# Optimization experiments

Hardware: AMD Instinct MI355X
Metric: run time of the kernel (lower is better)

The kernel has to match this reference:

```python
import jax, jax.numpy as jnp
import numpy as np

HIDDEN = 1024
FFN = 4 * HIDDEN
NUM_EXPERTS = 8
TOP_K = 2
B, S = 4, 2048


def setup_inputs() -> dict:
    key = jax.random.key(0)
    ks = jax.random.split(key, 7)
    scale = 0.02
    return {
        "x": jax.random.normal(ks[0], (B, S, HIDDEN), dtype=jnp.float32),
        "gate_w": jax.random.normal(ks[1], (HIDDEN, NUM_EXPERTS), dtype=jnp.float32) * scale,
        "gate_b": jnp.zeros((NUM_EXPERTS,), dtype=jnp.float32),
        "w1": jax.random.normal(ks[2], (NUM_EXPERTS, HIDDEN, FFN), dtype=jnp.float32) * scale,
        "b1": jnp.zeros((NUM_EXPERTS, FFN), dtype=jnp.float32),
        "w2": jax.random.normal(ks[3], (NUM_EXPERTS, FFN, HIDDEN), dtype=jnp.float32) * scale,
        "b2": jnp.zeros((NUM_EXPERTS, HIDDEN), dtype=jnp.float32),
    }


def reference(x, gate_w, gate_b, w1, b1, w2, b2):
    b, s, h = x.shape
    xt = x.reshape(b * s, h)  # [T, H]
    # gate: Linear + softmax
    probs = jax.nn.softmax(xt @ gate_w + gate_b, axis=-1)  # [T, E]
    _, idx = jax.lax.top_k(probs, TOP_K)  # [T, K] int32
    # one-hot over top-k -> boolean per-expert mask (matches original one_hot.sum>0)
    one_hot = jax.nn.one_hot(idx, NUM_EXPERTS, dtype=xt.dtype)  # [T, K, E]
    mask = (one_hot.sum(axis=1) > 0).astype(xt.dtype)  # [T, E]
    # every expert MLP applied to all tokens (dense equivalent of gather-MLP-scatter),
    # then masked combine: output[t] = sum_e mask[t,e] * MLP_e(x[t])
    h1 = jax.nn.relu(jnp.einsum('th,ehf->etf', xt, w1) + b1[:, None, :])  # [E, T, F]
    out_e = jnp.einsum('etf,efh->eth', h1, w2) + b2[:, None, :]  # [E, T, H]
    out = jnp.einsum('eth,te->th', out_e, mask)  # [T, H]
    return out.reshape(b, s, h)
```

## Files before the change

### kernel.cpp

```cpp
#include <hip/hip_runtime.h>

typedef __bf16 bf16_t;
typedef bf16_t bf16x8 __attribute__((ext_vector_type(8)));
typedef bf16_t bf16x4 __attribute__((ext_vector_type(4)));
typedef float floatx4 __attribute__((ext_vector_type(4)));

#define T_TOKENS 8192
#define HIDDEN 1024
#define FFN 4096
#define NE 8
#define PAIRS 16384
#define NTILES 136

#define GLD16(gp, lp) __builtin_amdgcn_global_load_lds( \
    (const __attribute__((address_space(1))) void*)(gp), \
    (__attribute__((address_space(3))) void*)(lp), 16, 0, 0)

__global__ __launch_bounds__(256) void gate_kernel(
    const float* __restrict__ x, const float* __restrict__ gw,
    const float* __restrict__ gb, unsigned* __restrict__ top2,
    int* __restrict__ counts)
{
    const int lane = threadIdx.x & 63;
    const int wid  = threadIdx.x >> 6;
    const int t    = blockIdx.x * 4 + wid;
    const float* xr = x + (size_t)t * HIDDEN;

    float s[NE];
#pragma unroll
    for (int e = 0; e < NE; ++e) s[e] = 0.f;
    for (int k = lane; k < HIDDEN; k += 64) {
        float xv = xr[k];
        const float* g = gw + (size_t)k * NE;
#pragma unroll
        for (int e = 0; e < NE; ++e) s[e] += xv * g[e];
    }
#pragma unroll
    for (int e = 0; e < NE; ++e) {
#pragma unroll
        for (int off = 32; off > 0; off >>= 1) s[e] += __shfl_xor(s[e], off, 64);
    }
    if (lane == 0) {
        float v1 = -1e30f, v2 = -1e30f;
        int i1 = 0, i2 = 0;
#pragma unroll
        for (int e = 0; e < NE; ++e) {
            float v = s[e] + gb[e];
            if (v > v1)      { v2 = v1; i2 = i1; v1 = v; i1 = e; }
            else if (v > v2) { v2 = v;  i2 = e; }
        }
        top2[t] = (unsigned)(i1 | (i2 << 4));
        atomicAdd(&counts[i1], 1);
        atomicAdd(&counts[i2], 1);
    }
}

__global__ void offsets_kernel(const int* __restrict__ counts,
                               int* __restrict__ offs,
                               int* __restrict__ tinfo)
{
    int acc = 0, nt = 0;
    for (int e = 0; e < NE; ++e) {
        offs[e] = acc;
        int n = counts[e];
        for (int r = 0; r < n; r += 128) tinfo[nt++] = e | ((r >> 7) << 4);
        acc += n;
    }
    for (; nt < NTILES; ++nt) tinfo[nt] = (65535 << 4);
}

__global__ __launch_bounds__(256) void scatter_kernel(
    unsigned* __restrict__ top2_slots, const int* __restrict__ offs,
    int* __restrict__ fill, unsigned short* __restrict__ tok16)
{
    const int t = blockIdx.x * 256 + threadIdx.x;
    const unsigned v = top2_slots[t];
    const int e1 = v & 15, e2 = (v >> 4) & 15;
    int p1 = atomicAdd(&fill[e1], 1);
    int s1 = offs[e1] + p1;
    tok16[s1] = (unsigned short)t;
    int p2 = atomicAdd(&fill[e2], 1);
    int s2 = offs[e2] + p2;
    tok16[s2] = (unsigned short)t;
    top2_slots[t] = (unsigned)s1 | ((unsigned)s2 << 16);
}

__global__ __launch_bounds__(256) void xconv_kernel(
    const float* __restrict__ x, bf16_t* __restrict__ xb)
{
    size_t i = ((size_t)blockIdx.x * 256 + threadIdx.x) * 4;
    float4 v = *(const float4*)(x + i);
    bf16x4 b;
    b[0] = (bf16_t)v.x; b[1] = (bf16_t)v.y; b[2] = (bf16_t)v.z; b[3] = (bf16_t)v.w;
    *(bf16x4*)(xb + i) = b;
}

__global__ __launch_bounds__(256) void wtrans_kernel(
    const float* __restrict__ in, bf16_t* __restrict__ out, int R, int C)
{
    __shared__ bf16_t L[64][68];
    const int e  = blockIdx.z;
    const int r0 = blockIdx.y * 64;
    const int c0 = blockIdx.x * 64;
    const float* ip = in + ((size_t)e * R + r0) * C + c0;
    bf16_t* op = out + ((size_t)e * C + c0) * R + r0;
    const int tid = threadIdx.x;
    const int lr = tid >> 4, lc4 = tid & 15;
#pragma unroll
    for (int p = 0; p < 4; ++p) {
        int r = p * 16 + lr;
        float4 v = *(const float4*)(ip + (size_t)r * C + lc4 * 4);
        bf16x4 b;
        b[0] = (bf16_t)v.x; b[1] = (bf16_t)v.y; b[2] = (bf16_t)v.z; b[3] = (bf16_t)v.w;
        *(bf16x4*)&L[r][lc4 * 4] = b;
    }
    __syncthreads();
#pragma unroll
    for (int p = 0; p < 4; ++p) {
        int c  = p * 16 + lr;
        int rr = lc4 * 4;
        bf16x4 b;
        b[0] = L[rr + 0][c]; b[1] = L[rr + 1][c];
        b[2] = L[rr + 2][c]; b[3] = L[rr + 3][c];
        *(bf16x4*)(op + (size_t)c * R + rr) = b;
    }
}

__global__ __launch_bounds__(256) void moe_gemm1(
    const bf16_t* __restrict__ xb, const bf16_t* __restrict__ w1t,
    const float* __restrict__ b1, const int* __restrict__ counts,
    const int* __restrict__ offs, const unsigned short* __restrict__ tok16,
    const int* __restrict__ tinfo, bf16_t* __restrict__ h1)
{
    const int info = tinfo[blockIdx.y];
    const int e    = info & 15;
    const int row0 = (info >> 4) << 7;
    const int n_e  = counts[e];
    if (row0 >= n_e) return;
    const int seg   = offs[e];
    const int fcol0 = blockIdx.x * 128;

    __shared__ bf16_t As[128 * 32];
    __shared__ bf16_t Bs[128 * 32];

    const int tid  = threadIdx.x;
    const int wid  = tid >> 6, lane = tid & 63;
    const int wm   = wid & 1,  wn   = wid >> 1;
    const int quad = lane >> 4, lrow = lane & 15;

    const bf16_t* pA[2]; const bf16_t* pB[2];
#pragma unroll
    for (int q = 0; q < 2; ++q) {
        int slot = q * 256 + tid;
        int arow = slot >> 2, ko = slot & 3;
        int ridx = row0 + arow; if (ridx > n_e - 1) ridx = n_e - 1;
        pA[q] = xb + (size_t)tok16[seg + ridx] * HIDDEN + ko * 8;
        pB[q] = w1t + ((size_t)e * FFN + fcol0 + arow) * HIDDEN + ko * 8;
    }

    floatx4 acc[4][4];
#pragma unroll
    for (int i = 0; i < 4; ++i)
#pragma unroll
        for (int j = 0; j < 4; ++j) acc[i][j] = (floatx4){0.f, 0.f, 0.f, 0.f};

    for (int k0 = 0; k0 < HIDDEN; k0 += 32) {
#pragma unroll
        for (int q = 0; q < 2; ++q) {
            GLD16(pA[q], As + (q * 256 + wid * 64) * 8);
            GLD16(pB[q], Bs + (q * 256 + wid * 64) * 8);
            pA[q] += 32; pB[q] += 32;
        }
        __syncthreads();
        bf16x8 af[4], bfr[4];
#pragma unroll
        for (int mi = 0; mi < 4; ++mi)
            af[mi] = *(const bf16x8*)&As[(wm * 64 + mi * 16 + lrow) * 32 + quad * 8];
#pragma unroll
        for (int ni = 0; ni < 4; ++ni)
            bfr[ni] = *(const bf16x8*)&Bs[(wn * 64 + ni * 16 + lrow) * 32 + quad * 8];
#pragma unroll
        for (int mi = 0; mi < 4; ++mi)
#pragma unroll
            for (int ni = 0; ni < 4; ++ni)
                acc[mi][ni] = __builtin_amdgcn_mfma_f32_16x16x32_bf16(
                    af[mi], bfr[ni], acc[mi][ni], 0, 0, 0);
        __syncthreads();
    }

#pragma unroll
    for (int ni = 0; ni < 4; ++ni) {
        const int col = wn * 64 + ni * 16 + lrow;
        const float bias = b1[(size_t)e * FFN + fcol0 + col];
#pragma unroll
        for (int mi = 0; mi < 4; ++mi) {
#pragma unroll
            for (int r = 0; r < 4; ++r) {
                int row = wm * 64 + mi * 16 + quad * 4 + r;
                if (row0 + row < n_e) {
                    float v = acc[mi][ni][r] + bias;
                    v = v > 0.f ? v : 0.f;
                    h1[(size_t)(seg + row0 + row) * FFN + fcol0 + col] = (bf16_t)v;
                }
            }
        }
    }
}

__global__ __launch_bounds__(256) void moe_gemm2(
    const bf16_t* __restrict__ h1, const bf16_t* __restrict__ w2t,
    const float* __restrict__ b2, const int* __restrict__ counts,
    const int* __restrict__ offs, const int* __restrict__ tinfo,
    float* __restrict__ out_pairs)
{
    const int info = tinfo[blockIdx.y];
    const int e    = info & 15;
    const int row0 = (info >> 4) << 7;
    const int n_e  = counts[e];
    if (row0 >= n_e) return;
    const int seg   = offs[e];
    const int hcol0 = blockIdx.x * 128;

    __shared__ bf16_t As[128 * 32];
    __shared__ bf16_t Bs[128 * 32];

    const int tid  = threadIdx.x;
    const int wid  = tid >> 6, lane = tid & 63;
    const int wm   = wid & 1,  wn   = wid >> 1;
    const int quad = lane >> 4, lrow = lane & 15;

    const bf16_t* pA[2]; const bf16_t* pB[2];
#pragma unroll
    for (int q = 0; q < 2; ++q) {
        int slot = q * 256 + tid;
        int arow = slot >> 2, ko = slot & 3;
        int ridx = row0 + arow; if (ridx > n_e - 1) ridx = n_e - 1;
        pA[q] = h1 + (size_t)(seg + ridx) * FFN + ko * 8;
        pB[q] = w2t + ((size_t)e * HIDDEN + hcol0 + arow) * FFN + ko * 8;
    }

    floatx4 acc[4][4];
#pragma unroll
    for (int i = 0; i < 4; ++i)
#pragma unroll
        for (int j = 0; j < 4; ++j) acc[i][j] = (floatx4){0.f, 0.f, 0.f, 0.f};

    for (int k0 = 0; k0 < FFN; k0 += 32) {
#pragma unroll
        for (int q = 0; q < 2; ++q) {
            GLD16(pA[q], As + (q * 256 + wid * 64) * 8);
            GLD16(pB[q], Bs + (q * 256 + wid * 64) * 8);
            pA[q] += 32; pB[q] += 32;
        }
        __syncthreads();
        bf16x8 af[4], bfr[4];
#pragma unroll
        for (int mi = 0; mi < 4; ++mi)
            af[mi] = *(const bf16x8*)&As[(wm * 64 + mi * 16 + lrow) * 32 + quad * 8];
#pragma unroll
        for (int ni = 0; ni < 4; ++ni)
            bfr[ni] = *(const bf16x8*)&Bs[(wn * 64 + ni * 16 + lrow) * 32 + quad * 8];
#pragma unroll
        for (int mi = 0; mi < 4; ++mi)
#pragma unroll
            for (int ni = 0; ni < 4; ++ni)
                acc[mi][ni] = __builtin_amdgcn_mfma_f32_16x16x32_bf16(
                    af[mi], bfr[ni], acc[mi][ni], 0, 0, 0);
        __syncthreads();
    }

#pragma unroll
    for (int ni = 0; ni < 4; ++ni) {
        const int col = wn * 64 + ni * 16 + lrow;
        const float bias = b2[(size_t)e * HIDDEN + hcol0 + col];
#pragma unroll
        for (int mi = 0; mi < 4; ++mi) {
#pragma unroll
            for (int r = 0; r < 4; ++r) {
                int row = wm * 64 + mi * 16 + quad * 4 + r;
                if (row0 + row < n_e) {
                    out_pairs[(size_t)(seg + row0 + row) * HIDDEN + hcol0 + col] =
                        acc[mi][ni][r] + bias;
                }
            }
        }
    }
}

__global__ __launch_bounds__(256) void combine_kernel(
    const float* __restrict__ op, const unsigned* __restrict__ slots,
    float* __restrict__ out)
{
    const int gid = blockIdx.x * 256 + threadIdx.x;
    const int t = gid >> 8;
    const int c = (gid & 255) * 4;
    const unsigned sv = slots[t];
    const int s1 = sv & 0xffff, s2 = sv >> 16;
    float4 a = *(const float4*)(op + (size_t)s1 * HIDDEN + c);
    float4 b = *(const float4*)(op + (size_t)s2 * HIDDEN + c);
    float4 o;
    o.x = a.x + b.x; o.y = a.y + b.y; o.z = a.z + b.z; o.w = a.w + b.w;
    *(float4*)(out + (size_t)t * HIDDEN + c) = o;
}

extern "C" void kernel_launch(void* const* d_in, const int* in_sizes, int n_in,
                              void* d_out, int out_size, void* d_ws, size_t ws_size,
                              hipStream_t stream)
{
    const float* x      = (const float*)d_in[0];
    const float* gate_w = (const float*)d_in[1];
    const float* gate_b = (const float*)d_in[2];
    const float* w1     = (const float*)d_in[3];
    const float* b1     = (const float*)d_in[4];
    const float* w2     = (const float*)d_in[5];
    const float* b2     = (const float*)d_in[6];
    float* out = (float*)d_out;

    char* ws = (char*)d_ws;
    int*      counts = (int*)(ws + 0);
    int*      fill   = (int*)(ws + 32);
    int*      offs   = (int*)(ws + 64);
    int*      tinfo  = (int*)(ws + 96);
    unsigned* top2   = (unsigned*)(ws + 640);
    unsigned short* tok16 = (unsigned short*)(ws + 640 + 32768);
    const size_t o_base = 98560;

    const size_t sz_xb  = (size_t)T_TOKENS * HIDDEN * 2;
    const size_t sz_w1t = (size_t)NE * FFN * HIDDEN * 2;
    const size_t sz_w2t = (size_t)NE * HIDDEN * FFN * 2;
    const size_t sz_h1  = (size_t)PAIRS * FFN * 2;
    const size_t need = o_base + sz_xb + sz_w1t + sz_w2t + sz_h1;
    if (ws_size < need) return;

    bf16_t* xb  = (bf16_t*)(ws + o_base);
    bf16_t* w1t = (bf16_t*)(ws + o_base + sz_xb);
    bf16_t* w2t = (bf16_t*)(ws + o_base + sz_xb + sz_w1t);
    bf16_t* h1  = (bf16_t*)(ws + o_base + sz_xb + sz_w1t + sz_w2t);
    float* out_pairs = (float*)w1t;

    hipMemsetAsync(ws, 0, 96, stream);

    gate_kernel<<<T_TOKENS / 4, 256, 0, stream>>>(x, gate_w, gate_b, top2, counts);
    offsets_kernel<<<1, 1, 0, stream>>>(counts, offs, tinfo);
    scatter_kernel<<<T_TOKENS / 256, 256, 0, stream>>>(top2, offs, fill, tok16);

    xconv_kernel<<<(T_TOKENS * HIDDEN) / 1024, 256, 0, stream>>>(x, xb);
    wtrans_kernel<<<dim3(FFN / 64, HIDDEN / 64, NE), 256, 0, stream>>>(w1, w1t, HIDDEN, FFN);
    wtrans_kernel<<<dim3(HIDDEN / 64, FFN / 64, NE), 256, 0, stream>>>(w2, w2t, FFN, HIDDEN);

    moe_gemm1<<<dim3(FFN / 128, NTILES), 256, 0, stream>>>(
        xb, w1t, b1, counts, offs, tok16, tinfo, h1);
    moe_gemm2<<<dim3(HIDDEN / 128, NTILES), 256, 0, stream>>>(
        h1, w2t, b2, counts, offs, tinfo, out_pairs);
    combine_kernel<<<(T_TOKENS * HIDDEN / 4) / 256, 256, 0, stream>>>(
        out_pairs, top2, out);
}
```

Measured before the change: 1.128 ms.

## Fuse x conversion into gate, widen GEMM K tile, swizzle LDS, atomic combine

The bf16 conversion of x moves into the gate kernel, and the separate combine kernel is dropped: gemm2 atomically adds biased results straight into a zeroed output. Both GEMMs use a 64-wide K tile with an XOR-swizzled LDS layout to reduce bank conflicts, a remapped block order that groups tiles for cache reuse, and a 3-blocks-per-CU launch bound. gemm1 now stages its output through LDS for 16-byte coalesced stores. The float atomics make the summation order nondeterministic and add a full memset of the output.

```diff
diff --git a/kernel.cpp b/kernel.cpp
--- a/kernel.cpp
+++ b/kernel.cpp
@@ -11,6 +11,7 @@
 #define NE 8
 #define PAIRS 16384
 #define NTILES 136
+#define BK 64
 
 #define GLD16(gp, lp) __builtin_amdgcn_global_load_lds( \
     (const __attribute__((address_space(1))) void*)(gp), \
@@ -19,21 +20,31 @@
 __global__ __launch_bounds__(256) void gate_kernel(
     const float* __restrict__ x, const float* __restrict__ gw,
     const float* __restrict__ gb, unsigned* __restrict__ top2,
-    int* __restrict__ counts)
+    int* __restrict__ counts, bf16_t* __restrict__ xb)
 {
     const int lane = threadIdx.x & 63;
     const int wid  = threadIdx.x >> 6;
     const int t    = blockIdx.x * 4 + wid;
-    const float* xr = x + (size_t)t * HIDDEN;
+    const float4* xr = (const float4*)(x + (size_t)t * HIDDEN);
+    bf16_t* xo = xb + (size_t)t * HIDDEN;
 
     float s[NE];
 #pragma unroll
     for (int e = 0; e < NE; ++e) s[e] = 0.f;
-    for (int k = lane; k < HIDDEN; k += 64) {
-        float xv = xr[k];
-        const float* g = gw + (size_t)k * NE;
-#pragma unroll
-        for (int e = 0; e < NE; ++e) s[e] += xv * g[e];
+#pragma unroll
+    for (int ii = 0; ii < 4; ++ii) {
+        const int i = ii * 64 + lane;
+        float4 v = xr[i];
+        bf16x4 b;
+        b[0] = (bf16_t)v.x; b[1] = (bf16_t)v.y; b[2] = (bf16_t)v.z; b[3] = (bf16_t)v.w;
+        *(bf16x4*)(xo + i * 4) = b;
+        const float* g = gw + (size_t)i * 32;
+#pragma unroll
+        for (int j = 0; j < 4; ++j) {
+            const float xv = (&v.x)[j];
+#pragma unroll
+            for (int e = 0; e < NE; ++e) s[e] += xv * g[j * 8 + e];
+        }
     }
 #pragma unroll
     for (int e = 0; e < NE; ++e) {
@@ -70,29 +81,14 @@
 }
 
 __global__ __launch_bounds__(256) void scatter_kernel(
-    unsigned* __restrict__ top2_slots, const int* __restrict__ offs,
+    const unsigned* __restrict__ top2, const int* __restrict__ offs,
     int* __restrict__ fill, unsigned short* __restrict__ tok16)
 {
     const int t = blockIdx.x * 256 + threadIdx.x;
-    const unsigned v = top2_slots[t];
+    const unsigned v = top2[t];
     const int e1 = v & 15, e2 = (v >> 4) & 15;
-    int p1 = atomicAdd(&fill[e1], 1);
-    int s1 = offs[e1] + p1;
-    tok16[s1] = (unsigned short)t;
-    int p2 = atomicAdd(&fill[e2], 1);
-    int s2 = offs[e2] + p2;
-    tok16[s2] = (unsigned short)t;
-    top2_slots[t] = (unsigned)s1 | ((unsigned)s2 << 16);
-}
-
-__global__ __launch_bounds__(256) void xconv_kernel(
-    const float* __restrict__ x, bf16_t* __restrict__ xb)
-{
-    size_t i = ((size_t)blockIdx.x * 256 + threadIdx.x) * 4;
-    float4 v = *(const float4*)(x + i);
-    bf16x4 b;
-    b[0] = (bf16_t)v.x; b[1] = (bf16_t)v.y; b[2] = (bf16_t)v.z; b[3] = (bf16_t)v.w;
-    *(bf16x4*)(xb + i) = b;
+    tok16[offs[e1] + atomicAdd(&fill[e1], 1)] = (unsigned short)t;
+    tok16[offs[e2] + atomicAdd(&fill[e2], 1)] = (unsigned short)t;
 }
 
 __global__ __launch_bounds__(256) void wtrans_kernel(
@@ -126,36 +122,45 @@
     }
 }
 
-__global__ __launch_bounds__(256) void moe_gemm1(
+__global__ __launch_bounds__(256, 3) void moe_gemm1(
     const bf16_t* __restrict__ xb, const bf16_t* __restrict__ w1t,
     const float* __restrict__ b1, const int* __restrict__ counts,
     const int* __restrict__ offs, const unsigned short* __restrict__ tok16,
     const int* __restrict__ tinfo, bf16_t* __restrict__ h1)
 {
-    const int info = tinfo[blockIdx.y];
+    const int nx = gridDim.x;
+    const int hw = blockIdx.y * nx + blockIdx.x;
+    const int chunk = (nx * gridDim.y) >> 3;
+    const int l  = (hw & 7) * chunk + (hw >> 3);
+    const int bx = l % nx;
+    const int by = l / nx;
+
+    const int info = tinfo[by];
     const int e    = info & 15;
     const int row0 = (info >> 4) << 7;
     const int n_e  = counts[e];
     if (row0 >= n_e) return;
     const int seg   = offs[e];
-    const int fcol0 = blockIdx.x * 128;
-
-    __shared__ bf16_t As[128 * 32];
-    __shared__ bf16_t Bs[128 * 32];
+    const int fcol0 = bx * 128;
+
+    __shared__ bf16_t S[128 * 128];
+    bf16_t* As = S;
+    bf16_t* Bs = S + 128 * BK;
 
     const int tid  = threadIdx.x;
     const int wid  = tid >> 6, lane = tid & 63;
     const int wm   = wid & 1,  wn   = wid >> 1;
     const int quad = lane >> 4, lrow = lane & 15;
 
-    const bf16_t* pA[2]; const bf16_t* pB[2];
-#pragma unroll
-    for (int q = 0; q < 2; ++q) {
+    const bf16_t* pA[4]; const bf16_t* pB[4];
+#pragma unroll
+    for (int q = 0; q < 4; ++q) {
         int slot = q * 256 + tid;
-        int arow = slot >> 2, ko = slot & 3;
+        int arow = slot >> 3, ko = slot & 7;
+        int kos  = ko ^ (arow & 7);
         int ridx = row0 + arow; if (ridx > n_e - 1) ridx = n_e - 1;
-        pA[q] = xb + (size_t)tok16[seg + ridx] * HIDDEN + ko * 8;
-        pB[q] = w1t + ((size_t)e * FFN + fcol0 + arow) * HIDDEN + ko * 8;
+        pA[q] = xb + (size_t)tok16[seg + ridx] * HIDDEN + kos * 8;
+        pB[q] = w1t + ((size_t)e * FFN + fcol0 + arow) * HIDDEN + kos * 8;
     }
 
     floatx4 acc[4][4];
@@ -164,27 +169,36 @@
 #pragma unroll
         for (int j = 0; j < 4; ++j) acc[i][j] = (floatx4){0.f, 0.f, 0.f, 0.f};
 
-    for (int k0 = 0; k0 < HIDDEN; k0 += 32) {
-#pragma unroll
-        for (int q = 0; q < 2; ++q) {
+    for (int k0 = 0; k0 < HIDDEN; k0 += BK) {
+#pragma unroll
+        for (int q = 0; q < 4; ++q) {
             GLD16(pA[q], As + (q * 256 + wid * 64) * 8);
             GLD16(pB[q], Bs + (q * 256 + wid * 64) * 8);
-            pA[q] += 32; pB[q] += 32;
+            pA[q] += BK; pB[q] += BK;
         }
         __syncthreads();
-        bf16x8 af[4], bfr[4];
-#pragma unroll
-        for (int mi = 0; mi < 4; ++mi)
-            af[mi] = *(const bf16x8*)&As[(wm * 64 + mi * 16 + lrow) * 32 + quad * 8];
-#pragma unroll
-        for (int ni = 0; ni < 4; ++ni)
-            bfr[ni] = *(const bf16x8*)&Bs[(wn * 64 + ni * 16 + lrow) * 32 + quad * 8];
-#pragma unroll
-        for (int mi = 0; mi < 4; ++mi)
-#pragma unroll
-            for (int ni = 0; ni < 4; ++ni)
-                acc[mi][ni] = __builtin_amdgcn_mfma_f32_16x16x32_bf16(
-                    af[mi], bfr[ni], acc[mi][ni], 0, 0, 0);
+#pragma unroll
+        for (int h = 0; h < 2; ++h) {
+            bf16x8 af[4], bfr[4];
+#pragma unroll
+            for (int mi = 0; mi < 4; ++mi) {
+                int r = wm * 64 + mi * 16 + lrow;
+                int g = (h * 4 + quad) ^ (r & 7);
+                af[mi] = *(const bf16x8*)&As[(r << 6) + (g << 3)];
+            }
+#pragma unroll
+            for (int ni = 0; ni < 4; ++ni) {
+                int r = wn * 64 + ni * 16 + lrow;
+                int g = (h * 4 + quad) ^ (r & 7);
+                bfr[ni] = *(const bf16x8*)&Bs[(r << 6) + (g << 3)];
+            }
+#pragma unroll
+            for (int mi = 0; mi < 4; ++mi)
+#pragma unroll
+                for (int ni = 0; ni < 4; ++ni)
+                    acc[mi][ni] = __builtin_amdgcn_mfma_f32_16x16x32_bf16(
+                        af[mi], bfr[ni], acc[mi][ni], 0, 0, 0);
+        }
         __syncthreads();
     }
 
@@ -193,50 +207,65 @@
         const int col = wn * 64 + ni * 16 + lrow;
         const float bias = b1[(size_t)e * FFN + fcol0 + col];
 #pragma unroll
-        for (int mi = 0; mi < 4; ++mi) {
+        for (int mi = 0; mi < 4; ++mi)
 #pragma unroll
             for (int r = 0; r < 4; ++r) {
                 int row = wm * 64 + mi * 16 + quad * 4 + r;
-                if (row0 + row < n_e) {
-                    float v = acc[mi][ni][r] + bias;
-                    v = v > 0.f ? v : 0.f;
-                    h1[(size_t)(seg + row0 + row) * FFN + fcol0 + col] = (bf16_t)v;
-                }
-            }
-        }
-    }
-}
-
-__global__ __launch_bounds__(256) void moe_gemm2(
+                float v = acc[mi][ni][r] + bias;
+                v = v > 0.f ? v : 0.f;
+                S[row * 128 + col] = (bf16_t)v;
+            }
+    }
+    __syncthreads();
+#pragma unroll
+    for (int i = 0; i < 8; ++i) {
+        int g16 = i * 256 + tid;
+        int row = g16 >> 4;
+        int ce  = (g16 & 15) * 8;
+        if (row0 + row < n_e)
+            *(bf16x8*)(h1 + (size_t)(seg + row0 + row) * FFN + fcol0 + ce) =
+                *(const bf16x8*)&S[row * 128 + ce];
+    }
+}
+
+__global__ __launch_bounds__(256, 3) void moe_gemm2(
     const bf16_t* __restrict__ h1, const bf16_t* __restrict__ w2t,
     const float* __restrict__ b2, const int* __restrict__ counts,
-    const int* __restrict__ offs, const int* __restrict__ tinfo,
-    float* __restrict__ out_pairs)
-{
-    const int info = tinfo[blockIdx.y];
+    const int* __restrict__ offs, const unsigned short* __restrict__ tok16,
+    const int* __restrict__ tinfo, float* __restrict__ out)
+{
+    const int nx = gridDim.x;
+    const int hw = blockIdx.y * nx + blockIdx.x;
+    const int chunk = (nx * gridDim.y) >> 3;
+    const int l  = (hw & 7) * chunk + (hw >> 3);
+    const int bx = l % nx;
+    const int by = l / nx;
+
+    const int info = tinfo[by];
     const int e    = info & 15;
     const int row0 = (info >> 4) << 7;
     const int n_e  = counts[e];
     if (row0 >= n_e) return;
     const int seg   = offs[e];
-    const int hcol0 = blockIdx.x * 128;
-
-    __shared__ bf16_t As[128 * 32];
-    __shared__ bf16_t Bs[128 * 32];
+    const int hcol0 = bx * 128;
+
+    __shared__ bf16_t As[128 * BK];
+    __shared__ bf16_t Bs[128 * BK];
 
     const int tid  = threadIdx.x;
     const int wid  = tid >> 6, lane = tid & 63;
     const int wm   = wid & 1,  wn   = wid >> 1;
     const int quad = lane >> 4, lrow = lane & 15;
 
-    const bf16_t* pA[2]; const bf16_t* pB[2];
-#pragma unroll
-    for (int q = 0; q < 2; ++q) {
+    const bf16_t* pA[4]; const bf16_t* pB[4];
+#pragma unroll
+    for (int q = 0; q < 4; ++q) {
         int slot = q * 256 + tid;
-        int arow = slot >> 2, ko = slot & 3;
+        int arow = slot >> 3, ko = slot & 7;
+        int kos  = ko ^ (arow & 7);
         int ridx = row0 + arow; if (ridx > n_e - 1) ridx = n_e - 1;
-        pA[q] = h1 + (size_t)(seg + ridx) * FFN + ko * 8;
-        pB[q] = w2t + ((size_t)e * HIDDEN + hcol0 + arow) * FFN + ko * 8;
+        pA[q] = h1 + (size_t)(seg + ridx) * FFN + kos * 8;
+        pB[q] = w2t + ((size_t)e * HIDDEN + hcol0 + arow) * FFN + kos * 8;
     }
 
     floatx4 acc[4][4];
@@ -245,62 +274,60 @@
 #pragma unroll
         for (int j = 0; j < 4; ++j) acc[i][j] = (floatx4){0.f, 0.f, 0.f, 0.f};
 
-    for (int k0 = 0; k0 < FFN; k0 += 32) {
-#pragma unroll
-        for (int q = 0; q < 2; ++q) {
+    for (int k0 = 0; k0 < FFN; k0 += BK) {
+#pragma unroll
+        for (int q = 0; q < 4; ++q) {
             GLD16(pA[q], As + (q * 256 + wid * 64) * 8);
             GLD16(pB[q], Bs + (q * 256 + wid * 64) * 8);
-            pA[q] += 32; pB[q] += 32;
+            pA[q] += BK; pB[q] += BK;
         }
         __syncthreads();
-        bf16x8 af[4], bfr[4];
-#pragma unroll
-        for (int mi = 0; mi < 4; ++mi)
-            af[mi] = *(const bf16x8*)&As[(wm * 64 + mi * 16 + lrow) * 32 + quad * 8];
-#pragma unroll
-        for (int ni = 0; ni < 4; ++ni)
-            bfr[ni] = *(const bf16x8*)&Bs[(wn * 64 + ni * 16 + lrow) * 32 + quad * 8];
-#pragma unroll
-        for (int mi = 0; mi < 4; ++mi)
-#pragma unroll
-            for (int ni = 0; ni < 4; ++ni)
-                acc[mi][ni] = __builtin_amdgcn_mfma_f32_16x16x32_bf16(
-                    af[mi], bfr[ni], acc[mi][ni], 0, 0, 0);
+#pragma unroll
+        for (int h = 0; h < 2; ++h) {
+            bf16x8 af[4], bfr[4];
+#pragma unroll
+            for (int mi = 0; mi < 4; ++mi) {
+                int r = wm * 64 + mi * 16 + lrow;
+                int g = (h * 4 + quad) ^ (r & 7);
+                af[mi] = *(const bf16x8*)&As[(r << 6) + (g << 3)];
+            }
+#pragma unroll
+            for (int ni = 0; ni < 4; ++ni) {
+                int r = wn * 64 + ni * 16 + lrow;
+                int g = (h * 4 + quad) ^ (r & 7);
+                bfr[ni] = *(const bf16x8*)&Bs[(r << 6) + (g << 3)];
+            }
+#pragma unroll
+            for (int mi = 0; mi < 4; ++mi)
+#pragma unroll
+                for (int ni = 0; ni < 4; ++ni)
+                    acc[mi][ni] = __builtin_amdgcn_mfma_f32_16x16x32_bf16(
+                        af[mi], bfr[ni], acc[mi][ni], 0, 0, 0);
+        }
         __syncthreads();
     }
 
+    int tokr[4][4];
+#pragma unroll
+    for (int mi = 0; mi < 4; ++mi)
+#pragma unroll
+        for (int r = 0; r < 4; ++r) {
+            int row = wm * 64 + mi * 16 + quad * 4 + r;
+            tokr[mi][r] = (row0 + row < n_e) ? (int)tok16[seg + row0 + row] : -1;
+        }
 #pragma unroll
     for (int ni = 0; ni < 4; ++ni) {
         const int col = wn * 64 + ni * 16 + lrow;
         const float bias = b2[(size_t)e * HIDDEN + hcol0 + col];
 #pragma unroll
-        for (int mi = 0; mi < 4; ++mi) {
+        for (int mi = 0; mi < 4; ++mi)
 #pragma unroll
             for (int r = 0; r < 4; ++r) {
-                int row = wm * 64 + mi * 16 + quad * 4 + r;
-                if (row0 + row < n_e) {
-                    out_pairs[(size_t)(seg + row0 + row) * HIDDEN + hcol0 + col] =
-                        acc[mi][ni][r] + bias;
-                }
-            }
-        }
-    }
-}
-
-__global__ __launch_bounds__(256) void combine_kernel(
-    const float* __restrict__ op, const unsigned* __restrict__ slots,
-    float* __restrict__ out)
-{
-    const int gid = blockIdx.x * 256 + threadIdx.x;
-    const int t = gid >> 8;
-    const int c = (gid & 255) * 4;
-    const unsigned sv = slots[t];
-    const int s1 = sv & 0xffff, s2 = sv >> 16;
-    float4 a = *(const float4*)(op + (size_t)s1 * HIDDEN + c);
-    float4 b = *(const float4*)(op + (size_t)s2 * HIDDEN + c);
-    float4 o;
-    o.x = a.x + b.x; o.y = a.y + b.y; o.z = a.z + b.z; o.w = a.w + b.w;
-    *(float4*)(out + (size_t)t * HIDDEN + c) = o;
+                if (tokr[mi][r] >= 0)
+                    atomicAdd(out + (size_t)tokr[mi][r] * HIDDEN + hcol0 + col,
+                              acc[mi][ni][r] + bias);
+            }
+    }
 }
 
 extern "C" void kernel_launch(void* const* d_in, const int* in_sizes, int n_in,
@@ -336,22 +363,19 @@
     bf16_t* w1t = (bf16_t*)(ws + o_base + sz_xb);
     bf16_t* w2t = (bf16_t*)(ws + o_base + sz_xb + sz_w1t);
     bf16_t* h1  = (bf16_t*)(ws + o_base + sz_xb + sz_w1t + sz_w2t);
-    float* out_pairs = (float*)w1t;
 
     hipMemsetAsync(ws, 0, 96, stream);
-
-    gate_kernel<<<T_TOKENS / 4, 256, 0, stream>>>(x, gate_w, gate_b, top2, counts);
+    hipMemsetAsync(out, 0, (size_t)T_TOKENS * HIDDEN * sizeof(float), stream);
+
+    gate_kernel<<<T_TOKENS / 4, 256, 0, stream>>>(x, gate_w, gate_b, top2, counts, xb);
     offsets_kernel<<<1, 1, 0, stream>>>(counts, offs, tinfo);
     scatter_kernel<<<T_TOKENS / 256, 256, 0, stream>>>(top2, offs, fill, tok16);
 
-    xconv_kernel<<<(T_TOKENS * HIDDEN) / 1024, 256, 0, stream>>>(x, xb);
     wtrans_kernel<<<dim3(FFN / 64, HIDDEN / 64, NE), 256, 0, stream>>>(w1, w1t, HIDDEN, FFN);
     wtrans_kernel<<<dim3(HIDDEN / 64, FFN / 64, NE), 256, 0, stream>>>(w2, w2t, FFN, HIDDEN);
 
     moe_gemm1<<<dim3(FFN / 128, NTILES), 256, 0, stream>>>(
         xb, w1t, b1, counts, offs, tok16, tinfo, h1);
     moe_gemm2<<<dim3(HIDDEN / 128, NTILES), 256, 0, stream>>>(
-        h1, w2t, b2, counts, offs, tinfo, out_pairs);
-    combine_kernel<<<(T_TOKENS * HIDDEN / 4) / 256, 256, 0, stream>>>(
-        out_pairs, top2, out);
-}
+        h1, w2t, b2, counts, offs, tok16, tinfo, out);
+}
```

Result: faster. 1.013 ms (-10.2%).
